# Kernel optimization log

Measured on AMD Instinct MI355X. Metric: run time of the kernel, lower is better.

## Reference

```python
import jax, jax.numpy as jnp
import numpy as np

E = 8            # n_expert
K = 2            # n_expert_per_token
C = 2048         # n_embd
I = 1408         # moe_intermediate_size
IS = I * 2       # shared expert intermediate (n_shared_expert=2)
B, T = 2, 2048


def setup_inputs() -> dict:
    key = jax.random.key(0)
    ks = jax.random.split(key, 9)
    s = 0.02
    return {
        "x": jax.random.normal(ks[0], (B, T, C), dtype=jnp.float32),
        "gate_w": jax.random.normal(ks[1], (E, C), dtype=jnp.float32) * s,
        # expert MLP weights, torch Linear convention (out_features, in_features)
        "w1": jax.random.normal(ks[2], (E, I, C), dtype=jnp.float32) * s,  # fc_1
        "w2": jax.random.normal(ks[3], (E, I, C), dtype=jnp.float32) * s,  # fc_2
        "w3": jax.random.normal(ks[4], (E, C, I), dtype=jnp.float32) * s,  # proj
        # shared expert
        "sw1": jax.random.normal(ks[5], (IS, C), dtype=jnp.float32) * s,
        "sw2": jax.random.normal(ks[6], (IS, C), dtype=jnp.float32) * s,
        "sw3": jax.random.normal(ks[7], (C, IS), dtype=jnp.float32) * s,
    }


def reference(x, gate_w, w1, w2, w3, sw1, sw2, sw3):
    Bq, Tq, Cq = x.shape
    xf = x.reshape(-1, Cq)  # [N, C], N = B*T

    # top-k routing: softmax in fp32, then top-k probs per token
    logits = xf @ gate_w.T                                   # [N, E]
    probs = jax.nn.softmax(logits.astype(jnp.float32), axis=-1)
    topk_p, topk_i = jax.lax.top_k(probs, K)                 # [N, K]
    # combine weights: comb[n, e] = sum_k topk_p[n,k] * (topk_i[n,k] == e)
    comb = (jax.nn.one_hot(topk_i, E, dtype=jnp.float32)
            * topk_p[..., None]).sum(axis=1).astype(x.dtype)  # [N, E]

    # per-expert gated-SiLU MLP (batched over experts via einsum)
    h1 = jnp.einsum('nc,eic->eni', xf, w1)                   # [E, N, I]
    h2 = jnp.einsum('nc,eic->eni', xf, w2)                   # [E, N, I]
    h = jax.nn.silu(h1) * h2
    eo = jnp.einsum('eni,eci->enc', h, w3)                   # [E, N, C]

    # weighted scatter-combine
    y = jnp.einsum('enc,ne->nc', eo, comb).reshape(Bq, Tq, Cq)

    # shared expert on the residual input
    sh = (jax.nn.silu(xf @ sw1.T) * (xf @ sw2.T)) @ sw3.T    # [N, C]
    return y + sh.reshape(Bq, Tq, Cq)
```

## Files before the change

### kernel.cpp

```cpp
#include <hip/hip_runtime.h>
#include <stdint.h>

#define N_TOK 4096
#define CDIM  2048
#define NEXP  8
#define IDIM  1408
#define ISDIM 2816
#define CAP   2048
#define ICAT  2816
#define SCAT  5632

typedef __attribute__((ext_vector_type(8))) short bf16x8;
typedef __attribute__((ext_vector_type(4))) float f32x4;

#define GLOAD16(gp, lp) __builtin_amdgcn_global_load_lds( \
    (const __attribute__((address_space(1))) void*)(gp),  \
    (__attribute__((address_space(3))) void*)(lp), 16, 0, 0)

__device__ __forceinline__ unsigned short f2bf(float f) {
  union { float f; unsigned u; } c; c.f = f;
  return (unsigned short)((c.u + 0x7FFFu + ((c.u >> 16) & 1u)) >> 16);
}
__device__ __forceinline__ float bf2f(unsigned short h) {
  union { unsigned u; float f; } c; c.u = (unsigned)h << 16;
  return c.f;
}

__device__ __forceinline__ int xcd_swizzle(int orig, int nwg) {
  int q = nwg >> 3, r = nwg & 7;
  int xcd = orig & 7, idx = orig >> 3;
  return (xcd < r ? xcd * (q + 1) : r * (q + 1) + (xcd - r) * q) + idx;
}

__global__ __launch_bounds__(256) void cvt_kernel(
    const float* __restrict__ s, unsigned short* __restrict__ d,
    int chunkElems, size_t dstOff, size_t dstStride) {
  size_t z = blockIdx.z;
  size_t i = (size_t)blockIdx.x * 1024 + (size_t)threadIdx.x * 4;
  if (i >= (size_t)chunkElems) return;
  float4 v = *(const float4*)(s + z * chunkElems + i);
  ushort4 o;
  o.x = f2bf(v.x); o.y = f2bf(v.y); o.z = f2bf(v.z); o.w = f2bf(v.w);
  *(ushort4*)(d + z * dstStride + dstOff + i) = o;
}

__global__ __launch_bounds__(64) void routing_kernel(
    const float* __restrict__ x, const float* __restrict__ gw,
    int* __restrict__ counts, int* __restrict__ list,
    int* __restrict__ slot_of, float* __restrict__ wts) {
  const int n = blockIdx.x;
  const int lane = threadIdx.x;
  const float* xr = x + (size_t)n * CDIM;
  float s[NEXP];
#pragma unroll
  for (int e = 0; e < NEXP; e++) s[e] = 0.f;
  for (int c = lane; c < CDIM; c += 64) {
    float xv = xr[c];
#pragma unroll
    for (int e = 0; e < NEXP; e++) s[e] += xv * gw[e * CDIM + c];
  }
#pragma unroll
  for (int e = 0; e < NEXP; e++) {
    float v = s[e];
    for (int o = 32; o > 0; o >>= 1) v += __shfl_down(v, o);
    s[e] = v;
  }
  if (lane == 0) {
    float mx = s[0];
#pragma unroll
    for (int e = 1; e < NEXP; e++) mx = fmaxf(mx, s[e]);
    float p[NEXP], sum = 0.f;
#pragma unroll
    for (int e = 0; e < NEXP; e++) { p[e] = __expf(s[e] - mx); sum += p[e]; }
    int i0 = 0;
#pragma unroll
    for (int e = 1; e < NEXP; e++) if (p[e] > p[i0]) i0 = e;
    int i1 = (i0 == 0) ? 1 : 0;
#pragma unroll
    for (int e = 0; e < NEXP; e++) if (e != i0 && p[e] > p[i1]) i1 = e;
    float inv = 1.f / sum;
    int s0 = atomicAdd(&counts[i0], 1);
    int s1 = atomicAdd(&counts[i1], 1);
    if (s0 < CAP) list[i0 * CAP + s0] = n; else s0 = 0;
    if (s1 < CAP) list[i1 * CAP + s1] = n; else s1 = 0;
    slot_of[n * 2]     = i0 * CAP + s0;
    slot_of[n * 2 + 1] = i1 * CAP + s1;
    wts[n * 2]     = p[i0] * inv;
    wts[n * 2 + 1] = p[i1] * inv;
  }
}

template <int PHASE>
__global__ __launch_bounds__(512) void moe_gemm(
    const unsigned short* __restrict__ xb,
    const unsigned short* __restrict__ swcat,
    const unsigned short* __restrict__ wcat,
    unsigned short* __restrict__ hsp,
    unsigned short* __restrict__ hep,
    const unsigned short* __restrict__ hs,
    const unsigned short* __restrict__ sw3b,
    const unsigned short* __restrict__ he,
    const unsigned short* __restrict__ w3b,
    float* __restrict__ ysf,
    unsigned short* __restrict__ eo,
    const int* __restrict__ list,
    const int* __restrict__ counts) {
  const int z = blockIdx.z;
  const unsigned short *A, *B;
  unsigned short* O = nullptr;
  float* Of = nullptr;
  int Ka, ldo;
  int cnt = 1 << 30;
  const int* lst = nullptr;
  int Mt, Nt;
  bool gath = false;
  if (PHASE == 1) {
    Mt = 8; Nt = 11; Ka = CDIM;
    if (z < 4) {
      int zm = z >> 1, zn = z & 1;
      A = xb + (size_t)zm * 2048 * CDIM;
      B = swcat + (size_t)zn * ISDIM * CDIM;
      O = hsp + (size_t)zm * 2048 * SCAT + (size_t)zn * ISDIM;
      ldo = SCAT;
    } else {
      int e = z - 4;
      cnt = counts[e]; if (cnt > CAP) cnt = CAP;
      lst = list + e * CAP;
      gath = true;
      A = xb;
      B = wcat + (size_t)e * ICAT * CDIM;
      O = hep + (size_t)e * CAP * ICAT;
      ldo = ICAT;
    }
  } else {
    Mt = 8; Nt = 8;
    if (z < 2) {
      Ka = ISDIM;
      A = hs + (size_t)z * 2048 * ISDIM;
      B = sw3b;
      Of = ysf + (size_t)z * 2048 * CDIM;
      ldo = CDIM;
    } else {
      int e = z - 2;
      cnt = counts[e]; if (cnt > CAP) cnt = CAP;
      Ka = IDIM;
      A = he + (size_t)e * CAP * IDIM;
      B = w3b + (size_t)e * CDIM * IDIM;
      O = eo + (size_t)e * CAP * CDIM;
      ldo = CDIM;
    }
  }
  const int wg = xcd_swizzle(blockIdx.x, Mt * Nt);
  const int mt = wg % Mt, nt = wg / Mt;
  if (mt * 256 >= cnt) return;

  __shared__ __align__(16) char lds[2][2][2][16384];

  const int tid = threadIdx.x;
  const int srow = tid >> 2;
  const int c16  = (tid & 3) << 4;
  const int scol = c16 ^ (((srow >> 1) & 3) << 4);
  const char* aS[2];
  const char* bS[2];
#pragma unroll
  for (int j = 0; j < 2; j++) {
    int ar = mt * 256 + j * 128 + srow;
    if (PHASE == 1 && gath) ar = (ar < cnt) ? lst[ar] : lst[0];
    aS[j] = (const char*)A + (size_t)ar * Ka * 2 + scol;
    int br = nt * 256 + j * 128 + srow;
    bS[j] = (const char*)B + (size_t)br * Ka * 2 + scol;
  }
  auto stageHalf = [&](int buf, int kt, int h) {
    size_t kb = (size_t)kt * 128 + (size_t)(h << 6);
    char* aD = &lds[buf][0][h][0] + tid * 16;
    char* bD = &lds[buf][1][h][0] + tid * 16;
    GLOAD16(aS[0] + kb, aD);
    GLOAD16(aS[1] + kb, aD + 8192);
    GLOAD16(bS[0] + kb, bD);
    GLOAD16(bS[1] + kb, bD + 8192);
  };

  const int lane = tid & 63, wid = tid >> 6;
  const int wr = wid >> 2, wc = wid & 3;
  const int lrow = lane & 15;
  const int klane = (lane >> 4) << 4;
  const int rsw = ((lrow >> 1) & 3) << 4;
  const int aOff = (wr * 128 + lrow) * 64 + (klane ^ rsw);
  const int bOff = (wc * 64 + lrow) * 64 + (klane ^ rsw);

  f32x4 acc[8][4];
#pragma unroll
  for (int mf = 0; mf < 8; mf++)
#pragma unroll
    for (int nf = 0; nf < 4; nf++) acc[mf][nf] = (f32x4){0.f, 0.f, 0.f, 0.f};

  stageHalf(0, 0, 0);
  stageHalf(0, 0, 1);
  stageHalf(1, 1, 0);
  asm volatile("s_waitcnt vmcnt(8)" ::: "memory");
  __builtin_amdgcn_s_barrier();

#define MFMA_Q(MB)                                                             \
  _Pragma("unroll")                                                            \
  for (int nf = 0; nf < 4; nf++)                                               \
    _Pragma("unroll")                                                          \
    for (int m = 0; m < 4; m++)                                                \
      acc[(MB) * 4 + m][nf] = __builtin_amdgcn_mfma_f32_16x16x32_bf16(         \
          aR[m], bR[nf], acc[(MB) * 4 + m][nf], 0, 0, 0);

  const int ntk = Ka >> 6;
  for (int t = 0; t < ntk; t++) {
    const int p = t & 1;
    const char* aK0 = &lds[p][0][0][0];
    const char* aK1 = &lds[p][0][1][0];
    const char* bK0 = &lds[p][1][0][0];
    const char* bK1 = &lds[p][1][1][0];
    bf16x8 aR[4], bR[4];
#pragma unroll
    for (int i = 0; i < 4; i++) aR[i] = *(const bf16x8*)(aK0 + aOff + i * 1024);
#pragma unroll
    for (int i = 0; i < 4; i++) bR[i] = *(const bf16x8*)(bK0 + bOff + i * 1024);
    if (t + 1 < ntk) stageHalf(p ^ 1, t + 1, 1);
    __builtin_amdgcn_s_barrier();
    asm volatile("s_waitcnt lgkmcnt(0)" ::: "memory");
    __builtin_amdgcn_s_setprio(1);
    MFMA_Q(0)
    __builtin_amdgcn_s_setprio(0);
    __builtin_amdgcn_s_barrier();
#pragma unroll
    for (int i = 0; i < 4; i++) aR[i] = *(const bf16x8*)(aK0 + aOff + (i + 4) * 1024);
    if (t + 1 < ntk) asm volatile("s_waitcnt vmcnt(8)" ::: "memory");
    else             asm volatile("s_waitcnt vmcnt(0)" ::: "memory");
    __builtin_amdgcn_s_barrier();
    asm volatile("s_waitcnt lgkmcnt(0)" ::: "memory");
    __builtin_amdgcn_s_setprio(1);
    MFMA_Q(1)
    __builtin_amdgcn_s_setprio(0);
    __builtin_amdgcn_s_barrier();
#pragma unroll
    for (int i = 0; i < 4; i++) aR[i] = *(const bf16x8*)(aK1 + aOff + i * 1024);
#pragma unroll
    for (int i = 0; i < 4; i++) bR[i] = *(const bf16x8*)(bK1 + bOff + i * 1024);
    if (t + 2 < ntk) stageHalf(p, t + 2, 0);
    __builtin_amdgcn_s_barrier();
    asm volatile("s_waitcnt lgkmcnt(0)" ::: "memory");
    __builtin_amdgcn_s_setprio(1);
    MFMA_Q(0)
    __builtin_amdgcn_s_setprio(0);
    __builtin_amdgcn_s_barrier();
#pragma unroll
    for (int i = 0; i < 4; i++) aR[i] = *(const bf16x8*)(aK1 + aOff + (i + 4) * 1024);
    if (t + 2 < ntk)      asm volatile("s_waitcnt vmcnt(8)" ::: "memory");
    else if (t + 1 < ntk) asm volatile("s_waitcnt vmcnt(4)" ::: "memory");
    __builtin_amdgcn_s_barrier();
    asm volatile("s_waitcnt lgkmcnt(0)" ::: "memory");
    __builtin_amdgcn_s_setprio(1);
    MFMA_Q(1)
    __builtin_amdgcn_s_setprio(0);
    __builtin_amdgcn_s_barrier();
  }
#undef MFMA_Q

  const int rowb = mt * 256 + wr * 128;
  const int colb = nt * 256 + wc * 64;
  const int r4 = (lane >> 4) * 4;
#pragma unroll
  for (int mf = 0; mf < 8; mf++) {
    int row0 = rowb + mf * 16 + r4;
#pragma unroll
    for (int nf = 0; nf < 4; nf++) {
      int col = colb + nf * 16 + lrow;
#pragma unroll
      for (int r = 0; r < 4; r++) {
        if (PHASE == 2 && z < 2)
          Of[(size_t)(row0 + r) * ldo + col] = acc[mf][nf][r];
        else
          O[(size_t)(row0 + r) * ldo + col] = f2bf(acc[mf][nf][r]);
      }
    }
  }
}

__global__ __launch_bounds__(256) void act_kernel(
    const unsigned short* __restrict__ in, unsigned short* __restrict__ out,
    int I8, int ldi) {
  int c8 = blockIdx.x * 256 + threadIdx.x;
  if (c8 >= I8) return;
  size_t r = blockIdx.y;
  const unsigned short* p = in + r * (size_t)ldi + (size_t)c8 * 8;
  bf16x8 a = *(const bf16x8*)p;
  bf16x8 g = *(const bf16x8*)(p + (size_t)I8 * 8);
  bf16x8 o;
#pragma unroll
  for (int k = 0; k < 8; k++) {
    float zv = bf2f((unsigned short)a[k]);
    float gv = bf2f((unsigned short)g[k]);
    float v = zv / (1.f + __expf(-zv)) * gv;
    o[k] = (short)f2bf(v);
  }
  *(bf16x8*)(out + r * (size_t)(I8 * 8) + (size_t)c8 * 8) = o;
}

__global__ __launch_bounds__(256) void combine_kernel(
    float* __restrict__ y, const float* __restrict__ ysf,
    const unsigned short* __restrict__ eo,
    const int* __restrict__ slot_of, const float* __restrict__ wts) {
  int idx = blockIdx.x * 256 + threadIdx.x;
  int n = idx >> 9;
  int c = (idx & 511) * 4;
  float4 v = *(const float4*)(ysf + (size_t)n * CDIM + c);
#pragma unroll
  for (int k = 0; k < 2; k++) {
    int slot = slot_of[n * 2 + k];
    float w = wts[n * 2 + k];
    ushort4 h = *(const ushort4*)(eo + (size_t)slot * CDIM + c);
    v.x += w * bf2f(h.x);
    v.y += w * bf2f(h.y);
    v.z += w * bf2f(h.z);
    v.w += w * bf2f(h.w);
  }
  *(float4*)(y + (size_t)n * CDIM + c) = v;
}

extern "C" void kernel_launch(void* const* d_in, const int* in_sizes, int n_in,
                              void* d_out, int out_size, void* d_ws, size_t ws_size,
                              hipStream_t stream) {
  const float* x   = (const float*)d_in[0];
  const float* gw  = (const float*)d_in[1];
  const float* w1  = (const float*)d_in[2];
  const float* w2  = (const float*)d_in[3];
  const float* w3  = (const float*)d_in[4];
  const float* sw1 = (const float*)d_in[5];
  const float* sw2 = (const float*)d_in[6];
  const float* sw3 = (const float*)d_in[7];
  float* y = (float*)d_out;

  char* ws = (char*)d_ws;
  size_t off = 0;
  auto alloc = [&](size_t b) -> void* {
    void* p = ws + off;
    off += (b + 255) & ~(size_t)255;
    return p;
  };
  unsigned short* xb    = (unsigned short*)alloc((size_t)N_TOK * CDIM * 2);
  unsigned short* wcat  = (unsigned short*)alloc((size_t)NEXP * ICAT * CDIM * 2);
  unsigned short* w3b   = (unsigned short*)alloc((size_t)NEXP * CDIM * IDIM * 2);
  unsigned short* swcat = (unsigned short*)alloc((size_t)SCAT * CDIM * 2);
  unsigned short* sw3b  = (unsigned short*)alloc((size_t)CDIM * ISDIM * 2);
  unsigned short* hsp   = (unsigned short*)alloc((size_t)N_TOK * SCAT * 2);
  unsigned short* hep   = (unsigned short*)alloc((size_t)NEXP * CAP * ICAT * 2);
  int*   counts  = (int*)alloc(NEXP * 4);
  int*   list    = (int*)alloc((size_t)NEXP * CAP * 4);
  int*   slot_of = (int*)alloc((size_t)N_TOK * 2 * 4);
  float* wtsb    = (float*)alloc((size_t)N_TOK * 2 * 4);
  unsigned short* hs = wcat;
  unsigned short* he = wcat + (size_t)N_TOK * ISDIM;
  float*          ysf = (float*)hsp;
  unsigned short* eoB = hep;

  hipMemsetAsync(counts, 0, NEXP * 4, stream);
  routing_kernel<<<N_TOK, 64, 0, stream>>>(x, gw, counts, list, slot_of, wtsb);

  cvt_kernel<<<dim3(8192, 1, 1), 256, 0, stream>>>(x, xb, N_TOK * CDIM, 0, 0);
  cvt_kernel<<<dim3(2816, 1, NEXP), 256, 0, stream>>>(w1, wcat, IDIM * CDIM, 0, (size_t)ICAT * CDIM);
  cvt_kernel<<<dim3(2816, 1, NEXP), 256, 0, stream>>>(w2, wcat, IDIM * CDIM, (size_t)IDIM * CDIM, (size_t)ICAT * CDIM);
  cvt_kernel<<<dim3(22528, 1, 1), 256, 0, stream>>>(w3, w3b, NEXP * CDIM * IDIM, 0, 0);
  cvt_kernel<<<dim3(5632, 1, 1), 256, 0, stream>>>(sw1, swcat, ISDIM * CDIM, 0, 0);
  cvt_kernel<<<dim3(5632, 1, 1), 256, 0, stream>>>(sw2, swcat, ISDIM * CDIM, (size_t)ISDIM * CDIM, 0);
  cvt_kernel<<<dim3(5632, 1, 1), 256, 0, stream>>>(sw3, sw3b, CDIM * ISDIM, 0, 0);

  moe_gemm<1><<<dim3(88, 1, 12), 512, 0, stream>>>(
      xb, swcat, wcat, hsp, hep, hs, sw3b, he, w3b, ysf, eoB, list, counts);

  act_kernel<<<dim3(2, N_TOK), 256, 0, stream>>>(hsp, hs, ISDIM / 8, SCAT);
  act_kernel<<<dim3(1, NEXP * CAP), 256, 0, stream>>>(hep, he, IDIM / 8, ICAT);

  moe_gemm<2><<<dim3(64, 1, 10), 512, 0, stream>>>(
      xb, swcat, wcat, hsp, hep, hs, sw3b, he, w3b, ysf, eoB, list, counts);

  combine_kernel<<<(N_TOK * (CDIM / 4)) / 256, 256, 0, stream>>>(y, ysf, eoB, slot_of, wtsb);
}
```

Before: 669.2 us.

## Fuse SiLU gating into first GEMM epilogue via interleaved gate/up weights

The fc_1 and fc_2 weight rows are interleaved in 128-row blocks during conversion, so each 256-wide output tile of the first GEMM holds matching gate and up columns. The epilogue exchanges one half through LDS and applies silu(z1)*z2 directly, writing only the half-width activation and dropping both act_kernel launches and the wide intermediate buffers. The seven conversion launches are merged into a single kernel. This adds an LDS round-trip and a barrier in the epilogue, and leaves half the waves idle while the output is written.

```diff
diff --git a/kernel.cpp b/kernel.cpp
--- a/kernel.cpp
+++ b/kernel.cpp
@@ -32,16 +32,55 @@
   return (xcd < r ? xcd * (q + 1) : r * (q + 1) + (xcd - r) * q) + idx;
 }
 
-__global__ __launch_bounds__(256) void cvt_kernel(
-    const float* __restrict__ s, unsigned short* __restrict__ d,
-    int chunkElems, size_t dstOff, size_t dstStride) {
-  size_t z = blockIdx.z;
-  size_t i = (size_t)blockIdx.x * 1024 + (size_t)threadIdx.x * 4;
-  if (i >= (size_t)chunkElems) return;
-  float4 v = *(const float4*)(s + z * chunkElems + i);
-  ushort4 o;
-  o.x = f2bf(v.x); o.y = f2bf(v.y); o.z = f2bf(v.z); o.w = f2bf(v.w);
-  *(ushort4*)(d + z * dstStride + dstOff + i) = o;
+__global__ __launch_bounds__(256) void cvt_all(
+    const float* __restrict__ x, const float* __restrict__ w1,
+    const float* __restrict__ w2, const float* __restrict__ w3,
+    const float* __restrict__ sw1, const float* __restrict__ sw2,
+    const float* __restrict__ sw3,
+    unsigned short* __restrict__ xb, unsigned short* __restrict__ wcat,
+    unsigned short* __restrict__ w3b, unsigned short* __restrict__ swcat,
+    unsigned short* __restrict__ sw3b) {
+  const int b = blockIdx.x;
+  const int t = threadIdx.x;
+  const float* src;
+  unsigned short* dst;
+  if (b < 4096) {
+    src = x + (size_t)b * 2048;  dst = xb + (size_t)b * 2048;
+  } else if (b < 15360) {
+    size_t o = (size_t)(b - 4096) * 2048;  src = w3 + o;  dst = w3b + o;
+  } else if (b < 18176) {
+    size_t o = (size_t)(b - 15360) * 2048; src = sw3 + o; dst = sw3b + o;
+  } else if (b < 40704) {
+    int g = b - 18176;
+    int e = g / 2816, r = g - e * 2816;
+    int dr;
+    if (r < 1408) { src = w1 + ((size_t)e * 1408 + r) * 2048; dr = (r >> 7) * 256 + (r & 127); }
+    else { int r2 = r - 1408; src = w2 + ((size_t)e * 1408 + r2) * 2048; dr = (r2 >> 7) * 256 + 128 + (r2 & 127); }
+    dst = wcat + ((size_t)e * ICAT + dr) * 2048;
+  } else {
+    int g = b - 40704;
+    int dr;
+    if (g < 2816) {
+      int zn = g >= 1408, rr = g - zn * 1408;
+      src = sw1 + (size_t)g * 2048;
+      dr = zn * 2816 + (rr >> 7) * 256 + (rr & 127);
+    } else {
+      int r = g - 2816;
+      int zn = r >= 1408, rr = r - zn * 1408;
+      src = sw2 + (size_t)r * 2048;
+      dr = zn * 2816 + (rr >> 7) * 256 + 128 + (rr & 127);
+    }
+    dst = swcat + (size_t)dr * 2048;
+  }
+  size_t i = (size_t)t * 8;
+  float4 v0 = *(const float4*)(src + i);
+  float4 v1 = *(const float4*)(src + i + 4);
+  bf16x8 o;
+  o[0] = (short)f2bf(v0.x); o[1] = (short)f2bf(v0.y);
+  o[2] = (short)f2bf(v0.z); o[3] = (short)f2bf(v0.w);
+  o[4] = (short)f2bf(v1.x); o[5] = (short)f2bf(v1.y);
+  o[6] = (short)f2bf(v1.z); o[7] = (short)f2bf(v1.w);
+  *(bf16x8*)(dst + i) = o;
 }
 
 __global__ __launch_bounds__(64) void routing_kernel(
@@ -95,8 +134,8 @@
     const unsigned short* __restrict__ xb,
     const unsigned short* __restrict__ swcat,
     const unsigned short* __restrict__ wcat,
-    unsigned short* __restrict__ hsp,
-    unsigned short* __restrict__ hep,
+    unsigned short* __restrict__ hs_out,
+    unsigned short* __restrict__ he_out,
     const unsigned short* __restrict__ hs,
     const unsigned short* __restrict__ sw3b,
     const unsigned short* __restrict__ he,
@@ -119,9 +158,9 @@
     if (z < 4) {
       int zm = z >> 1, zn = z & 1;
       A = xb + (size_t)zm * 2048 * CDIM;
-      B = swcat + (size_t)zn * ISDIM * CDIM;
-      O = hsp + (size_t)zm * 2048 * SCAT + (size_t)zn * ISDIM;
-      ldo = SCAT;
+      B = swcat + (size_t)zn * 2816 * CDIM;
+      O = hs_out + (size_t)zm * 2048 * ISDIM + (size_t)zn * 1408;
+      ldo = ISDIM;
     } else {
       int e = z - 4;
       cnt = counts[e]; if (cnt > CAP) cnt = CAP;
@@ -129,8 +168,8 @@
       gath = true;
       A = xb;
       B = wcat + (size_t)e * ICAT * CDIM;
-      O = hep + (size_t)e * CAP * ICAT;
-      ldo = ICAT;
+      O = he_out + (size_t)e * CAP * IDIM;
+      ldo = IDIM;
     }
   } else {
     Mt = 8; Nt = 8;
@@ -261,44 +300,61 @@
   }
 #undef MFMA_Q
 
-  const int rowb = mt * 256 + wr * 128;
-  const int colb = nt * 256 + wc * 64;
   const int r4 = (lane >> 4) * 4;
-#pragma unroll
-  for (int mf = 0; mf < 8; mf++) {
-    int row0 = rowb + mf * 16 + r4;
-#pragma unroll
-    for (int nf = 0; nf < 4; nf++) {
-      int col = colb + nf * 16 + lrow;
-#pragma unroll
-      for (int r = 0; r < 4; r++) {
-        if (PHASE == 2 && z < 2)
-          Of[(size_t)(row0 + r) * ldo + col] = acc[mf][nf][r];
-        else
-          O[(size_t)(row0 + r) * ldo + col] = f2bf(acc[mf][nf][r]);
+  if (PHASE == 1) {
+    float* ldsF = (float*)&lds[0][0][0][0];
+    const int rbase = wr * 128 + r4;
+    if (wc >= 2) {
+      const int cb = (wc - 2) * 64;
+#pragma unroll
+      for (int mf = 0; mf < 8; mf++)
+#pragma unroll
+        for (int nf = 0; nf < 4; nf++) {
+          int cc = cb + nf * 16 + lrow;
+#pragma unroll
+          for (int r = 0; r < 4; r++)
+            ldsF[(rbase + mf * 16 + r) * 128 + cc] = acc[mf][nf][r];
+        }
+    }
+    __syncthreads();
+    if (wc < 2) {
+      const int cb = wc * 64;
+#pragma unroll
+      for (int mf = 0; mf < 8; mf++) {
+        int row0 = mt * 256 + wr * 128 + mf * 16 + r4;
+#pragma unroll
+        for (int nf = 0; nf < 4; nf++) {
+          int cc = cb + nf * 16 + lrow;
+          int col = nt * 128 + cc;
+#pragma unroll
+          for (int r = 0; r < 4; r++) {
+            float z1 = acc[mf][nf][r];
+            float z2 = ldsF[(rbase + mf * 16 + r) * 128 + cc];
+            float gv = z1 / (1.f + __expf(-z1)) * z2;
+            O[(size_t)(row0 + r) * ldo + col] = f2bf(gv);
+          }
+        }
       }
     }
-  }
-}
-
-__global__ __launch_bounds__(256) void act_kernel(
-    const unsigned short* __restrict__ in, unsigned short* __restrict__ out,
-    int I8, int ldi) {
-  int c8 = blockIdx.x * 256 + threadIdx.x;
-  if (c8 >= I8) return;
-  size_t r = blockIdx.y;
-  const unsigned short* p = in + r * (size_t)ldi + (size_t)c8 * 8;
-  bf16x8 a = *(const bf16x8*)p;
-  bf16x8 g = *(const bf16x8*)(p + (size_t)I8 * 8);
-  bf16x8 o;
-#pragma unroll
-  for (int k = 0; k < 8; k++) {
-    float zv = bf2f((unsigned short)a[k]);
-    float gv = bf2f((unsigned short)g[k]);
-    float v = zv / (1.f + __expf(-zv)) * gv;
-    o[k] = (short)f2bf(v);
-  }
-  *(bf16x8*)(out + r * (size_t)(I8 * 8) + (size_t)c8 * 8) = o;
+  } else {
+    const int rowb = mt * 256 + wr * 128;
+    const int colb = nt * 256 + wc * 64;
+#pragma unroll
+    for (int mf = 0; mf < 8; mf++) {
+      int row0 = rowb + mf * 16 + r4;
+#pragma unroll
+      for (int nf = 0; nf < 4; nf++) {
+        int col = colb + nf * 16 + lrow;
+#pragma unroll
+        for (int r = 0; r < 4; r++) {
+          if (z < 2)
+            Of[(size_t)(row0 + r) * ldo + col] = acc[mf][nf][r];
+          else
+            O[(size_t)(row0 + r) * ldo + col] = f2bf(acc[mf][nf][r]);
+        }
+      }
+    }
+  }
 }
 
 __global__ __launch_bounds__(256) void combine_kernel(
@@ -347,36 +403,26 @@
   unsigned short* w3b   = (unsigned short*)alloc((size_t)NEXP * CDIM * IDIM * 2);
   unsigned short* swcat = (unsigned short*)alloc((size_t)SCAT * CDIM * 2);
   unsigned short* sw3b  = (unsigned short*)alloc((size_t)CDIM * ISDIM * 2);
-  unsigned short* hsp   = (unsigned short*)alloc((size_t)N_TOK * SCAT * 2);
-  unsigned short* hep   = (unsigned short*)alloc((size_t)NEXP * CAP * ICAT * 2);
+  unsigned short* hs    = (unsigned short*)alloc((size_t)N_TOK * ISDIM * 2);
+  unsigned short* he    = (unsigned short*)alloc((size_t)NEXP * CAP * IDIM * 2);
+  float*          ysf   = (float*)alloc((size_t)N_TOK * CDIM * 4);
   int*   counts  = (int*)alloc(NEXP * 4);
   int*   list    = (int*)alloc((size_t)NEXP * CAP * 4);
   int*   slot_of = (int*)alloc((size_t)N_TOK * 2 * 4);
   float* wtsb    = (float*)alloc((size_t)N_TOK * 2 * 4);
-  unsigned short* hs = wcat;
-  unsigned short* he = wcat + (size_t)N_TOK * ISDIM;
-  float*          ysf = (float*)hsp;
-  unsigned short* eoB = hep;
+  unsigned short* eoB = wcat;
 
   hipMemsetAsync(counts, 0, NEXP * 4, stream);
   routing_kernel<<<N_TOK, 64, 0, stream>>>(x, gw, counts, list, slot_of, wtsb);
 
-  cvt_kernel<<<dim3(8192, 1, 1), 256, 0, stream>>>(x, xb, N_TOK * CDIM, 0, 0);
-  cvt_kernel<<<dim3(2816, 1, NEXP), 256, 0, stream>>>(w1, wcat, IDIM * CDIM, 0, (size_t)ICAT * CDIM);
-  cvt_kernel<<<dim3(2816, 1, NEXP), 256, 0, stream>>>(w2, wcat, IDIM * CDIM, (size_t)IDIM * CDIM, (size_t)ICAT * CDIM);
-  cvt_kernel<<<dim3(22528, 1, 1), 256, 0, stream>>>(w3, w3b, NEXP * CDIM * IDIM, 0, 0);
-  cvt_kernel<<<dim3(5632, 1, 1), 256, 0, stream>>>(sw1, swcat, ISDIM * CDIM, 0, 0);
-  cvt_kernel<<<dim3(5632, 1, 1), 256, 0, stream>>>(sw2, swcat, ISDIM * CDIM, (size_t)ISDIM * CDIM, 0);
-  cvt_kernel<<<dim3(5632, 1, 1), 256, 0, stream>>>(sw3, sw3b, CDIM * ISDIM, 0, 0);
+  cvt_all<<<46336, 256, 0, stream>>>(x, w1, w2, w3, sw1, sw2, sw3,
+                                     xb, wcat, w3b, swcat, sw3b);
 
   moe_gemm<1><<<dim3(88, 1, 12), 512, 0, stream>>>(
-      xb, swcat, wcat, hsp, hep, hs, sw3b, he, w3b, ysf, eoB, list, counts);
-
-  act_kernel<<<dim3(2, N_TOK), 256, 0, stream>>>(hsp, hs, ISDIM / 8, SCAT);
-  act_kernel<<<dim3(1, NEXP * CAP), 256, 0, stream>>>(hep, he, IDIM / 8, ICAT);
+      xb, swcat, wcat, hs, he, hs, sw3b, he, w3b, ysf, eoB, list, counts);
 
   moe_gemm<2><<<dim3(64, 1, 10), 512, 0, stream>>>(
-      xb, swcat, wcat, hsp, hep, hs, sw3b, he, w3b, ysf, eoB, list, counts);
+      xb, swcat, wcat, hs, he, hs, sw3b, he, w3b, ysf, eoB, list, counts);
 
   combine_kernel<<<(N_TOK * (CDIM / 4)) / 256, 256, 0, stream>>>(y, ysf, eoB, slot_of, wtsb);
 }
```

Result: faster. 631.3 us (-5.7%).
